# Kernel optimization log

Hardware: AMD Instinct MI355X
Metric: run time of the kernel (lower is better)

The kernel has to match this reference:

```python
import jax, jax.numpy as jnp
import numpy as np

B, S, H = 16, 4096, 768
NUM_WORDS = S // 2  # 2048: max distinct words per sample (padded output width)


def setup_inputs() -> dict:
    key = jax.random.key(0)
    k1, k2 = jax.random.split(key)
    hidden_states = jax.random.normal(k1, (B, S, H), dtype=jnp.float32)
    # word ids: non-decreasing, contiguous from 0; -1 marks special tokens (None in HF)
    inc = jax.random.bernoulli(k2, 0.5, (B, S)).astype(jnp.int32)
    inc = inc.at[:, :2].set(0)  # keep word 0 alive at position 1 after masking CLS
    word_ids = jnp.maximum(jnp.cumsum(inc, axis=1) - 1, 0)
    word_ids = jnp.minimum(word_ids, NUM_WORDS - 1)  # static cap on segment count
    word_ids = word_ids.at[:, 0].set(-1)   # [CLS]
    word_ids = word_ids.at[:, -1].set(-1)  # [SEP]
    return {"hidden_states": hidden_states, "word_ids": word_ids}


def reference(hidden_states, word_ids):
    # Segment-mean of subword embeddings into word embeddings.
    # hidden_states: [B, S, H] float; word_ids: [B, S] int, -1 = special token (dropped).
    b, s, h = hidden_states.shape
    valid = word_ids >= 0  # [B, S]
    # offset per-sample word ids into a flat segment space of size B*NUM_WORDS;
    # invalid tokens go to segment (b*NUM_WORDS + 0) but contribute zeros.
    wid = jnp.where(valid, word_ids, 0)
    seg = (wid + jnp.arange(b, dtype=word_ids.dtype)[:, None] * NUM_WORDS).reshape(-1)
    data = jnp.where(valid[..., None], hidden_states, 0.0).reshape(b * s, h)
    sums = jax.ops.segment_sum(data, seg, num_segments=b * NUM_WORDS)
    counts = jax.ops.segment_sum(
        valid.reshape(-1).astype(hidden_states.dtype), seg, num_segments=b * NUM_WORDS
    )
    sums = sums.reshape(b, NUM_WORDS, h)
    counts = counts.reshape(b, NUM_WORDS)
    # mean per word; words with zero tokens stay 0 (matches pad_sequence zero-padding)
    return sums / jnp.maximum(counts, 1.0)[..., None]
```

## Files before the change

### kernel.cpp

```cpp
#include <hip/hip_runtime.h>

constexpr int B = 16;
constexpr int S = 4096;
constexpr int H = 768;
constexpr int NW = 2048;
constexpr int V4 = H / 4;
constexpr int T = 32;
constexpr int CPS = 128;
constexpr int WAVES_PER_BLK = 4;

__device__ __forceinline__ void acc4(float4& a, const float4 v) {
    a.x += v.x; a.y += v.y; a.z += v.z; a.w += v.w;
}

__global__ __launch_bounds__(256)
void seg_mean_kernel(const float* __restrict__ hs,
                     const int* __restrict__ wid,
                     float* __restrict__ out) {
    const int wave = threadIdx.x >> 6;
    const int lane = threadIdx.x & 63;
    const int gc = blockIdx.x * WAVES_PER_BLK + wave;
    const int b = gc >> 7;
    const int chunk = gc & (CPS - 1);
    const int t0 = 1 + chunk * T;

    const int* __restrict__ wrow = wid + (size_t)b * S;

    int gidx = t0 - 1 + lane;
    if (gidx > S - 1) gidx = S - 1;
    if (lane == 63) gidx = S - 2;
    const int wv = wrow[gidx];

    const float4* __restrict__ base = (const float4*)(hs + (size_t)b * S * H);

#define SLOTS(X) X(0) X(1) X(2) X(3) X(4) X(5) X(6) X(7)
#define DECLP(J) float4 pA##J, pB##J, pC##J;
#define DECLQ(J) float4 qA##J, qB##J, qC##J;
    SLOTS(DECLP)
    SLOTS(DECLQ)

#define LOAD1(R, J, TB) { int t = (TB) + J; if (t > S - 2) t = S - 2;      \
        const float4* p = base + (size_t)t * V4;                           \
        R##A##J = p[lane]; R##B##J = p[lane + 64]; R##C##J = p[lane + 128]; }
#define ISSUE(R, TB) LOAD1(R,0,TB) LOAD1(R,1,TB) LOAD1(R,2,TB) LOAD1(R,3,TB) \
                     LOAD1(R,4,TB) LOAD1(R,5,TB) LOAD1(R,6,TB) LOAD1(R,7,TB)

    ISSUE(p, t0)
    ISSUE(q, t0 + 8)
    __builtin_amdgcn_sched_barrier(0);

    const int maxw = __builtin_amdgcn_readlane(wv, 63);

    const int wprev = __shfl_up(wv, 1);
    const bool chg = (lane >= 1) && (lane <= 62) && (wv != wprev);
    const unsigned long long mask = __ballot(chg);

    const float4 z = make_float4(0.f, 0.f, 0.f, 0.f);
    float4 a0 = z, a1 = z, a2 = z;
    int cnt = 0, wcur = 0;
    bool active = false;

    auto flush = [&]() {
        const float inv = 1.0f / (float)cnt;
        float4 m0 = a0, m1 = a1, m2 = a2;
        m0.x *= inv; m0.y *= inv; m0.z *= inv; m0.w *= inv;
        m1.x *= inv; m1.y *= inv; m1.z *= inv; m1.w *= inv;
        m2.x *= inv; m2.y *= inv; m2.z *= inv; m2.w *= inv;
        float4* o = (float4*)(out + ((size_t)b * NW + wcur) * H);
        o[lane] = m0; o[lane + 64] = m1; o[lane + 128] = m2;
    };

#define STEPX(BIT, RA, RB, RC) {                                           \
        if ((mask >> (BIT)) & 1ull) {                                      \
            if (active) flush();                                           \
            const int wval = __builtin_amdgcn_readlane(wv, (BIT));         \
            active = (wval >= 0);                                          \
            if (active) { wcur = wval; a0 = z; a1 = z; a2 = z; cnt = 0; }  \
        }                                                                  \
        if (active) { acc4(a0, RA); acc4(a1, RB); acc4(a2, RC); ++cnt; } }
#define CONSUME(BB, R) \
    STEPX((BB)+1, R##A0, R##B0, R##C0) STEPX((BB)+2, R##A1, R##B1, R##C1)  \
    STEPX((BB)+3, R##A2, R##B2, R##C2) STEPX((BB)+4, R##A3, R##B3, R##C3)  \
    STEPX((BB)+5, R##A4, R##B4, R##C4) STEPX((BB)+6, R##A5, R##B5, R##C5)  \
    STEPX((BB)+7, R##A6, R##B6, R##C6) STEPX((BB)+8, R##A7, R##B7, R##C7)

    CONSUME(0, p)
    ISSUE(p, t0 + 16)
    __builtin_amdgcn_sched_barrier(0);
    CONSUME(8, q)
    ISSUE(q, t0 + 24)
    __builtin_amdgcn_sched_barrier(0);
    CONSUME(16, p)
    CONSUME(24, q)
#undef CONSUME
#undef STEPX
#undef ISSUE
#undef LOAD1
#undef DECLP
#undef DECLQ
#undef SLOTS

    if (active) {
        int end;
        const unsigned long long hi = mask >> 33;
        if (hi) {
            end = t0 + 32 + __builtin_ctzll(hi);
        } else {
            end = t0 + 62;
            while (true) {
                int t = end + lane;
                if (t > S - 1) t = S - 1;
                const int wv2 = wrow[t];
                const unsigned long long m2 = __ballot(wv2 != wcur);
                if (m2) { end += __builtin_ctzll(m2); break; }
                end += 64;
            }
        }
        cnt += end - (t0 + 32);
        int t = t0 + 32;
        for (; t + 3 < end; t += 4) {
            const float4* p0 = base + (size_t)t * V4;
            const float4* p1 = p0 + V4;
            const float4* p2 = p1 + V4;
            const float4* p3 = p2 + V4;
            float4 x00 = p0[lane], x01 = p0[lane + 64], x02 = p0[lane + 128];
            float4 x10 = p1[lane], x11 = p1[lane + 64], x12 = p1[lane + 128];
            float4 x20 = p2[lane], x21 = p2[lane + 64], x22 = p2[lane + 128];
            float4 x30 = p3[lane], x31 = p3[lane + 64], x32 = p3[lane + 128];
            acc4(a0, x00); acc4(a1, x01); acc4(a2, x02);
            acc4(a0, x10); acc4(a1, x11); acc4(a2, x12);
            acc4(a0, x20); acc4(a1, x21); acc4(a2, x22);
            acc4(a0, x30); acc4(a1, x31); acc4(a2, x32);
        }
        for (; t < end; ++t) {
            const float4* p = base + (size_t)t * V4;
            float4 v0 = p[lane], v1 = p[lane + 64], v2 = p[lane + 128];
            acc4(a0, v0); acc4(a1, v1); acc4(a2, v2);
        }
        flush();
    }

    {
        const int wz0 = chunk * 16;
#pragma unroll
        for (int k = 0; k < 16; ++k) {
            const int w = wz0 + k;
            if (w > maxw) {
                float4* o = (float4*)(out + ((size_t)b * NW + w) * H);
                o[lane] = z; o[lane + 64] = z; o[lane + 128] = z;
            }
        }
    }
}

extern "C" void kernel_launch(void* const* d_in, const int* in_sizes, int n_in,
                              void* d_out, int out_size, void* d_ws, size_t ws_size,
                              hipStream_t stream) {
    const float* hs = (const float*)d_in[0];
    const int* wid = (const int*)d_in[1];
    float* out = (float*)d_out;

    seg_mean_kernel<<<(B * CPS) / WAVES_PER_BLK, 64 * WAVES_PER_BLK, 0, stream>>>(
        hs, wid, out);
}
```

Before: 312.2 us.

## Make segment accumulation branchless with predicated stores to a dummy buffer

Replaces the per-token branchy flush/reset logic with branchless selects. The accumulators are reset through an FMA by a 0/1 keep factor, and every step stores its mean either to the real output row or to a scratch row in the workspace. It also shrinks the prefetch groups from 8 tokens to 4 tokens per register set and adds a launch-bounds occupancy hint of 2. The aim is to remove divergent scalar branching and register pressure, at the cost of issuing a full 3-float4 store per token, most of which go to dummy memory and add write traffic.

```diff
diff --git a/kernel.cpp b/kernel.cpp
--- a/kernel.cpp
+++ b/kernel.cpp
@@ -13,10 +13,11 @@
     a.x += v.x; a.y += v.y; a.z += v.z; a.w += v.w;
 }
 
-__global__ __launch_bounds__(256)
+__global__ __launch_bounds__(256, 2)
 void seg_mean_kernel(const float* __restrict__ hs,
                      const int* __restrict__ wid,
-                     float* __restrict__ out) {
+                     float* __restrict__ out,
+                     float* __restrict__ ws) {
     const int wave = threadIdx.x >> 6;
     const int lane = threadIdx.x & 63;
     const int gc = blockIdx.x * WAVES_PER_BLK + wave;
@@ -32,112 +33,136 @@
     const int wv = wrow[gidx];
 
     const float4* __restrict__ base = (const float4*)(hs + (size_t)b * S * H);
+    float4* __restrict__ outb = (float4*)out;
+    float4* const dummy = (float4*)ws + (size_t)(gc & 31) * V4;
+    const int ob = b * NW;
 
-#define SLOTS(X) X(0) X(1) X(2) X(3) X(4) X(5) X(6) X(7)
-#define DECLP(J) float4 pA##J, pB##J, pC##J;
-#define DECLQ(J) float4 qA##J, qB##J, qC##J;
-    SLOTS(DECLP)
-    SLOTS(DECLQ)
+#define GDECL(P) float4 P##0,P##1,P##2,P##3,P##4,P##5,P##6,P##7,P##8,P##9,P##10,P##11;
+    GDECL(pA)
+    GDECL(pB)
+#define LD1(P, K, TT) { int t = (TT); if (t > S - 2) t = S - 2;            \
+        const float4* p = base + (size_t)t * V4;                           \
+        P##K = p[lane]; }
+#define GISSUE(P, TB)                                                      \
+    { int t=(TB);   if(t>S-2)t=S-2; const float4* p=base+(size_t)t*V4;     \
+      P##0=p[lane]; P##1=p[lane+64]; P##2=p[lane+128]; }                   \
+    { int t=(TB)+1; if(t>S-2)t=S-2; const float4* p=base+(size_t)t*V4;     \
+      P##3=p[lane]; P##4=p[lane+64]; P##5=p[lane+128]; }                   \
+    { int t=(TB)+2; if(t>S-2)t=S-2; const float4* p=base+(size_t)t*V4;     \
+      P##6=p[lane]; P##7=p[lane+64]; P##8=p[lane+128]; }                   \
+    { int t=(TB)+3; if(t>S-2)t=S-2; const float4* p=base+(size_t)t*V4;     \
+      P##9=p[lane]; P##10=p[lane+64]; P##11=p[lane+128]; }
 
-#define LOAD1(R, J, TB) { int t = (TB) + J; if (t > S - 2) t = S - 2;      \
-        const float4* p = base + (size_t)t * V4;                           \
-        R##A##J = p[lane]; R##B##J = p[lane + 64]; R##C##J = p[lane + 128]; }
-#define ISSUE(R, TB) LOAD1(R,0,TB) LOAD1(R,1,TB) LOAD1(R,2,TB) LOAD1(R,3,TB) \
-                     LOAD1(R,4,TB) LOAD1(R,5,TB) LOAD1(R,6,TB) LOAD1(R,7,TB)
-
-    ISSUE(p, t0)
-    ISSUE(q, t0 + 8)
+    GISSUE(pA, t0)
+    GISSUE(pB, t0 + 4)
     __builtin_amdgcn_sched_barrier(0);
 
     const int maxw = __builtin_amdgcn_readlane(wv, 63);
-
     const int wprev = __shfl_up(wv, 1);
     const bool chg = (lane >= 1) && (lane <= 62) && (wv != wprev);
     const unsigned long long mask = __ballot(chg);
 
     const float4 z = make_float4(0.f, 0.f, 0.f, 0.f);
     float4 a0 = z, a1 = z, a2 = z;
-    int cnt = 0, wcur = 0;
-    bool active = false;
+    bool valid = false;
+    int cnt = 0;
+    int wval = -1;
+    float4* wptr = dummy;
 
-    auto flush = [&]() {
+#define STEP(J, RA, RB, RC) {                                              \
+    const bool bnd = (mask >> ((J) + 1)) & 1ull;                           \
+    const int wvj = __builtin_amdgcn_readlane(wv, (J) + 1);                \
+    float4* const wcand = outb + (size_t)(ob + (wvj & (NW - 1))) * V4;     \
+    wptr = bnd ? wcand : wptr;                                             \
+    valid = bnd ? (wvj >= 0) : valid;                                      \
+    wval = bnd ? wvj : wval;                                               \
+    cnt = bnd ? 1 : cnt + 1;                                               \
+    const float keep = bnd ? 0.0f : 1.0f;                                  \
+    a0.x = fmaf(a0.x, keep, RA.x); a0.y = fmaf(a0.y, keep, RA.y);          \
+    a0.z = fmaf(a0.z, keep, RA.z); a0.w = fmaf(a0.w, keep, RA.w);          \
+    a1.x = fmaf(a1.x, keep, RB.x); a1.y = fmaf(a1.y, keep, RB.y);          \
+    a1.z = fmaf(a1.z, keep, RB.z); a1.w = fmaf(a1.w, keep, RB.w);          \
+    a2.x = fmaf(a2.x, keep, RC.x); a2.y = fmaf(a2.y, keep, RC.y);          \
+    a2.z = fmaf(a2.z, keep, RC.z); a2.w = fmaf(a2.w, keep, RC.w);          \
+    const bool is_last = (mask >> ((J) + 2)) & 1ull;                       \
+    const float inv = 1.0f / (float)cnt;                                   \
+    float4 m0, m1, m2;                                                     \
+    m0.x=a0.x*inv; m0.y=a0.y*inv; m0.z=a0.z*inv; m0.w=a0.w*inv;            \
+    m1.x=a1.x*inv; m1.y=a1.y*inv; m1.z=a1.z*inv; m1.w=a1.w*inv;            \
+    m2.x=a2.x*inv; m2.y=a2.y*inv; m2.z=a2.z*inv; m2.w=a2.w*inv;            \
+    float4* const sp = (is_last && valid) ? wptr : dummy;                  \
+    sp[lane] = m0; sp[lane + 64] = m1; sp[lane + 128] = m2; }
+
+#define GCONSUME(P, JB)                                                    \
+    STEP((JB) + 0, P##0, P##1, P##2)                                       \
+    STEP((JB) + 1, P##3, P##4, P##5)                                       \
+    STEP((JB) + 2, P##6, P##7, P##8)                                       \
+    STEP((JB) + 3, P##9, P##10, P##11)
+
+    GCONSUME(pA, 0)
+    GISSUE(pA, t0 + 8)
+    __builtin_amdgcn_sched_barrier(0);
+    GCONSUME(pB, 4)
+    GISSUE(pB, t0 + 12)
+    __builtin_amdgcn_sched_barrier(0);
+    GCONSUME(pA, 8)
+    GISSUE(pA, t0 + 16)
+    __builtin_amdgcn_sched_barrier(0);
+    GCONSUME(pB, 12)
+    GISSUE(pB, t0 + 20)
+    __builtin_amdgcn_sched_barrier(0);
+    GCONSUME(pA, 16)
+    GISSUE(pA, t0 + 24)
+    __builtin_amdgcn_sched_barrier(0);
+    GCONSUME(pB, 20)
+    GISSUE(pB, t0 + 28)
+    __builtin_amdgcn_sched_barrier(0);
+    GCONSUME(pA, 24)
+    GCONSUME(pB, 28)
+#undef GCONSUME
+#undef STEP
+#undef GISSUE
+#undef LD1
+#undef GDECL
+
+    const bool closed = (mask >> 33) & 1ull;
+    if (valid && !closed) {
+        int end_excl;
+        const unsigned long long sh = (mask & 0x7fffffffffffffffull) >> 34;
+        if (sh) {
+            end_excl = t0 + 33 + __builtin_ctzll(sh);
+        } else {
+            int probe = t0 + 62;
+            while (true) {
+                int tt = probe + lane;
+                if (tt > S - 1) tt = S - 1;
+                const int w2 = wrow[tt];
+                const unsigned long long mm = __ballot(w2 != wval);
+                if (mm) { end_excl = probe + __builtin_ctzll(mm); break; }
+                probe += 64;
+            }
+        }
+        cnt += end_excl - (t0 + 32);
+        int t = t0 + 32;
+        for (; t + 1 < end_excl; t += 2) {
+            const float4* p0 = base + (size_t)t * V4;
+            const float4* p1 = p0 + V4;
+            float4 v0 = p0[lane], v1 = p0[lane + 64], v2 = p0[lane + 128];
+            float4 u0 = p1[lane], u1 = p1[lane + 64], u2 = p1[lane + 128];
+            acc4(a0, v0); acc4(a1, v1); acc4(a2, v2);
+            acc4(a0, u0); acc4(a1, u1); acc4(a2, u2);
+        }
+        if (t < end_excl) {
+            const float4* p = base + (size_t)t * V4;
+            float4 v0 = p[lane], v1 = p[lane + 64], v2 = p[lane + 128];
+            acc4(a0, v0); acc4(a1, v1); acc4(a2, v2);
+        }
         const float inv = 1.0f / (float)cnt;
         float4 m0 = a0, m1 = a1, m2 = a2;
         m0.x *= inv; m0.y *= inv; m0.z *= inv; m0.w *= inv;
         m1.x *= inv; m1.y *= inv; m1.z *= inv; m1.w *= inv;
         m2.x *= inv; m2.y *= inv; m2.z *= inv; m2.w *= inv;
-        float4* o = (float4*)(out + ((size_t)b * NW + wcur) * H);
-        o[lane] = m0; o[lane + 64] = m1; o[lane + 128] = m2;
-    };
-
-#define STEPX(BIT, RA, RB, RC) {                                           \
-        if ((mask >> (BIT)) & 1ull) {                                      \
-            if (active) flush();                                           \
-            const int wval = __builtin_amdgcn_readlane(wv, (BIT));         \
-            active = (wval >= 0);                                          \
-            if (active) { wcur = wval; a0 = z; a1 = z; a2 = z; cnt = 0; }  \
-        }                                                                  \
-        if (active) { acc4(a0, RA); acc4(a1, RB); acc4(a2, RC); ++cnt; } }
-#define CONSUME(BB, R) \
-    STEPX((BB)+1, R##A0, R##B0, R##C0) STEPX((BB)+2, R##A1, R##B1, R##C1)  \
-    STEPX((BB)+3, R##A2, R##B2, R##C2) STEPX((BB)+4, R##A3, R##B3, R##C3)  \
-    STEPX((BB)+5, R##A4, R##B4, R##C4) STEPX((BB)+6, R##A5, R##B5, R##C5)  \
-    STEPX((BB)+7, R##A6, R##B6, R##C6) STEPX((BB)+8, R##A7, R##B7, R##C7)
-
-    CONSUME(0, p)
-    ISSUE(p, t0 + 16)
-    __builtin_amdgcn_sched_barrier(0);
-    CONSUME(8, q)
-    ISSUE(q, t0 + 24)
-    __builtin_amdgcn_sched_barrier(0);
-    CONSUME(16, p)
-    CONSUME(24, q)
-#undef CONSUME
-#undef STEPX
-#undef ISSUE
-#undef LOAD1
-#undef DECLP
-#undef DECLQ
-#undef SLOTS
-
-    if (active) {
-        int end;
-        const unsigned long long hi = mask >> 33;
-        if (hi) {
-            end = t0 + 32 + __builtin_ctzll(hi);
-        } else {
-            end = t0 + 62;
-            while (true) {
-                int t = end + lane;
-                if (t > S - 1) t = S - 1;
-                const int wv2 = wrow[t];
-                const unsigned long long m2 = __ballot(wv2 != wcur);
-                if (m2) { end += __builtin_ctzll(m2); break; }
-                end += 64;
-            }
-        }
-        cnt += end - (t0 + 32);
-        int t = t0 + 32;
-        for (; t + 3 < end; t += 4) {
-            const float4* p0 = base + (size_t)t * V4;
-            const float4* p1 = p0 + V4;
-            const float4* p2 = p1 + V4;
-            const float4* p3 = p2 + V4;
-            float4 x00 = p0[lane], x01 = p0[lane + 64], x02 = p0[lane + 128];
-            float4 x10 = p1[lane], x11 = p1[lane + 64], x12 = p1[lane + 128];
-            float4 x20 = p2[lane], x21 = p2[lane + 64], x22 = p2[lane + 128];
-            float4 x30 = p3[lane], x31 = p3[lane + 64], x32 = p3[lane + 128];
-            acc4(a0, x00); acc4(a1, x01); acc4(a2, x02);
-            acc4(a0, x10); acc4(a1, x11); acc4(a2, x12);
-            acc4(a0, x20); acc4(a1, x21); acc4(a2, x22);
-            acc4(a0, x30); acc4(a1, x31); acc4(a2, x32);
-        }
-        for (; t < end; ++t) {
-            const float4* p = base + (size_t)t * V4;
-            float4 v0 = p[lane], v1 = p[lane + 64], v2 = p[lane + 128];
-            acc4(a0, v0); acc4(a1, v1); acc4(a2, v2);
-        }
-        flush();
+        wptr[lane] = m0; wptr[lane + 64] = m1; wptr[lane + 128] = m2;
     }
 
     {
@@ -146,7 +171,7 @@
         for (int k = 0; k < 16; ++k) {
             const int w = wz0 + k;
             if (w > maxw) {
-                float4* o = (float4*)(out + ((size_t)b * NW + w) * H);
+                float4* o = outb + (size_t)(ob + w) * V4;
                 o[lane] = z; o[lane + 64] = z; o[lane + 128] = z;
             }
         }
@@ -159,7 +184,8 @@
     const float* hs = (const float*)d_in[0];
     const int* wid = (const int*)d_in[1];
     float* out = (float*)d_out;
+    float* ws = (float*)d_ws;
 
     seg_mean_kernel<<<(B * CPS) / WAVES_PER_BLK, 64 * WAVES_PER_BLK, 0, stream>>>(
-        hs, wid, out);
+        hs, wid, out, ws);
 }
```

Measured after the change: 320.4 us. 2.6% more time.
